# Optimization experiments

Measured on AMD Instinct MI355X. Metric: run time of the kernel, lower is better.

Reference implementation:

```python
import jax, jax.numpy as jnp
import numpy as np

ENC, TAG, LANG, ATT = 512, 512, 512, 256
N, P = 1024, 1024


def setup_inputs() -> dict:
    key = jax.random.key(0)
    ks = jax.random.split(key, 11)
    s = lambda d: 1.0 / np.sqrt(d)
    return {
        "encoder_out": jax.random.normal(ks[0], (1, P, ENC), jnp.float32),
        "decoder_hidden": jax.random.normal(ks[1], (N, TAG), jnp.float32),
        "language_out": jax.random.normal(ks[2], (N, LANG), jnp.float32),
        "We": jax.random.uniform(ks[3], (ATT, ENC), jnp.float32, -s(ENC), s(ENC)),
        "be": jax.random.uniform(ks[4], (ATT,), jnp.float32, -s(ENC), s(ENC)),
        "Wt": jax.random.uniform(ks[5], (ATT, TAG), jnp.float32, -s(TAG), s(TAG)),
        "bt": jax.random.uniform(ks[6], (ATT,), jnp.float32, -s(TAG), s(TAG)),
        "Wl": jax.random.uniform(ks[7], (ATT, LANG), jnp.float32, -s(LANG), s(LANG)),
        "bl": jax.random.uniform(ks[8], (ATT,), jnp.float32, -s(LANG), s(LANG)),
        "Wf": jax.random.uniform(ks[9], (1, ATT), jnp.float32, -s(ATT), s(ATT)),
        "bf": jax.random.uniform(ks[10], (1,), jnp.float32, -s(ATT), s(ATT)),
    }


def reference(encoder_out, decoder_hidden, language_out, We, be, Wt, bt, Wl, bl, Wf, bf):
    # att1: (1, P, A); att2, att3: (N, A)
    att1 = jnp.einsum("bpe,ae->bpa", encoder_out, We) + be
    att2 = decoder_hidden @ Wt.T + bt
    att3 = language_out @ Wl.T + bl
    # broadcast add -> (N, P, A), relu, reduce to scalar score per pixel
    h = jax.nn.relu(att1 + (att2 + att3)[:, None, :])  # (N, P, A)
    att = jnp.einsum("npa,a->np", h, Wf[0]) + bf[0]     # (N, P)
    alpha = jax.nn.softmax(att, axis=1)
    # softmax-weighted sum over pixels -> (N, ENC)
    awe = jnp.einsum("np,pe->ne", alpha, encoder_out[0])
    return awe, alpha
```

## Files before the change

### kernel.cpp

```cpp
#include <hip/hip_runtime.h>
#include <hip/hip_bf16.h>
#include <math.h>

#define ENC 512
#define ATT 256
#define NN 1024
#define PP 1024

typedef __attribute__((ext_vector_type(8))) __bf16 bf16x8;
typedef __attribute__((ext_vector_type(4))) float floatx4;
typedef __attribute__((ext_vector_type(2))) float floatx2;

union LdsVec { uint4 u; bf16x8 v; };

__device__ __forceinline__ unsigned cvt_pk(float lo, float hi) {
    union { __hip_bfloat162 h; unsigned u; } x;
    x.h = __float22bfloat162_rn(float2{lo, hi});
    return x.u;
}
__device__ __forceinline__ uint4 cvt8(float4 f0, float4 f1) {
    uint4 r;
    r.x = cvt_pk(f0.x, f0.y); r.y = cvt_pk(f0.z, f0.w);
    r.z = cvt_pk(f1.x, f1.y); r.w = cvt_pk(f1.z, f1.w);
    return r;
}
__device__ __forceinline__ float2 bfpair(unsigned w) {
    union { unsigned u; float f; } lo, hi;
    lo.u = w << 16; hi.u = w & 0xffff0000u;
    return float2{lo.f, hi.f};
}

__device__ __forceinline__ int tile_off(int row, int k) {
    return row * 32 + ((((k >> 3) ^ ((row >> 1) & 3)) & 3) << 3) + (k & 7);
}

__global__ __launch_bounds__(256) void mfma_uv(
    const float* __restrict__ E,  const float* __restrict__ We, const float* __restrict__ be,
    const float* __restrict__ D,  const float* __restrict__ Wt, const float* __restrict__ bt,
    const float* __restrict__ Lg, const float* __restrict__ Wl, const float* __restrict__ bl,
    unsigned short* __restrict__ uT, unsigned short* __restrict__ v1T,
    unsigned short* __restrict__ v2T, unsigned short* __restrict__ ET,
    float* __restrict__ S)
{
    const int tid = threadIdx.x;

    if (blockIdx.z == 3) {
        if (blockIdx.x == 0 && blockIdx.y == 0) {
            const floatx4 z4 = {0.f, 0.f, 0.f, 0.f};
            *(floatx4*)&S[tid * 4] = z4;
        }
        __shared__ unsigned short T[64][72];
        const int k0 = blockIdx.y * 64;
        const int kr = tid >> 2, nc = (tid & 3) * 16;
        const int nr = tid >> 2, kc = (tid & 3) * 16;
        #pragma unroll
        for (int t = 0; t < 2; ++t) {
            const int n0 = (blockIdx.x * 2 + t) * 64;
            const float* ep = E + (size_t)(k0 + kr) * ENC + n0 + nc;
            float4 a = *(const float4*)(ep + 0),  b = *(const float4*)(ep + 4);
            float4 c = *(const float4*)(ep + 8),  d = *(const float4*)(ep + 12);
            if (t) __syncthreads();
            *(uint4*)&T[kr][nc]     = cvt8(a, b);
            *(uint4*)&T[kr][nc + 8] = cvt8(c, d);
            __syncthreads();
            unsigned short tmp[16];
            #pragma unroll
            for (int i = 0; i < 16; ++i) tmp[i] = T[kc + i][nr];
            unsigned short* op = ET + (size_t)(n0 + nr) * PP + k0 + kc;
            *(uint4*)(op)     = *(uint4*)&tmp[0];
            *(uint4*)(op + 8) = *(uint4*)&tmp[8];
        }
        return;
    }

    __shared__ __align__(16) unsigned short As[2][64 * 32];
    __shared__ __align__(16) unsigned short Bs[2][64 * 32];
    const int K = 512;

    const float *A, *B, *bias; unsigned short* out;
    if      (blockIdx.z == 0) { A = E;  B = We; bias = be; out = uT;  }
    else if (blockIdx.z == 1) { A = D;  B = Wt; bias = bt; out = v1T; }
    else                      { A = Lg; B = Wl; bias = bl; out = v2T; }

    const int m0 = blockIdx.y * 64, n0 = blockIdx.x * 64;
    const int wv = tid >> 6, lm = tid & 15, lq = (tid >> 4) & 3;
    const int mb = (wv & 1) * 32, nb = (wv >> 1) * 32;
    const int a0o = tile_off(mb + lm,      lq * 8);
    const int a1o = tile_off(mb + 16 + lm, lq * 8);
    const int b0o = tile_off(nb + lm,      lq * 8);
    const int b1o = tile_off(nb + 16 + lm, lq * 8);

    const int row = tid >> 2, kseg = tid & 3;
    const int soff = tile_off(row, kseg * 8);
    const float* Ap = A + (size_t)(m0 + row) * K + kseg * 8;
    const float* Bp = B + (size_t)(n0 + row) * K + kseg * 8;

    floatx4 acc[2][2];
    const floatx4 zero = {0.f, 0.f, 0.f, 0.f};
    acc[0][0] = zero; acc[0][1] = zero; acc[1][0] = zero; acc[1][1] = zero;

    float4 pa0 = *(const float4*)(Ap), pa1 = *(const float4*)(Ap + 4);
    float4 pb0 = *(const float4*)(Bp), pb1 = *(const float4*)(Bp + 4);

    for (int k0 = 0; k0 < K; k0 += 32) {
        const int buf = (k0 >> 5) & 1;
        *(uint4*)&As[buf][soff] = cvt8(pa0, pa1);
        *(uint4*)&Bs[buf][soff] = cvt8(pb0, pb1);
        __syncthreads();
        if (k0 + 32 < K) {
            pa0 = *(const float4*)(Ap + k0 + 32); pa1 = *(const float4*)(Ap + k0 + 36);
            pb0 = *(const float4*)(Bp + k0 + 32); pb1 = *(const float4*)(Bp + k0 + 36);
        }
        LdsVec fa0, fa1, fb0, fb1;
        fa0.u = *(const uint4*)&As[buf][a0o];
        fa1.u = *(const uint4*)&As[buf][a1o];
        fb0.u = *(const uint4*)&Bs[buf][b0o];
        fb1.u = *(const uint4*)&Bs[buf][b1o];
        acc[0][0] = __builtin_amdgcn_mfma_f32_16x16x32_bf16(fa0.v, fb0.v, acc[0][0], 0, 0, 0);
        acc[0][1] = __builtin_amdgcn_mfma_f32_16x16x32_bf16(fa0.v, fb1.v, acc[0][1], 0, 0, 0);
        acc[1][0] = __builtin_amdgcn_mfma_f32_16x16x32_bf16(fa1.v, fb0.v, acc[1][0], 0, 0, 0);
        acc[1][1] = __builtin_amdgcn_mfma_f32_16x16x32_bf16(fa1.v, fb1.v, acc[1][1], 0, 0, 0);
    }

    #pragma unroll
    for (int s = 0; s < 2; ++s) {
        const int col = n0 + nb + s * 16 + lm;
        const float bsum = bias[col];
        #pragma unroll
        for (int t = 0; t < 2; ++t) {
            const int mbase = m0 + mb + t * 16 + lq * 4;
            uint2 o;
            o.x = cvt_pk(acc[t][s][0] + bsum, acc[t][s][1] + bsum);
            o.y = cvt_pk(acc[t][s][2] + bsum, acc[t][s][3] + bsum);
            *(uint2*)&out[(size_t)col * NN + mbase] = o;
        }
    }
}

__global__ __launch_bounds__(256) void att_exp(
    const unsigned short* __restrict__ uT, const unsigned short* __restrict__ v1T,
    const unsigned short* __restrict__ v2T,
    const float* __restrict__ Wf,
    unsigned short* __restrict__ expv, float* __restrict__ S)
{
    __shared__ float us[32][68];
    __shared__ float vs[32][68];
    __shared__ float wfs[ATT];
    const int tid = threadIdx.x;
    wfs[tid] = Wf[tid];
    const int p0 = blockIdx.x * 64, n0 = blockIdx.y * 64;
    const int rowS = tid >> 3, cS = (tid & 7) * 8;
    const int tx = tid & 15, ty = tid >> 4;

    floatx2 acc[4][2];
    const floatx2 z2 = {0.f, 0.f};
    #pragma unroll
    for (int j = 0; j < 4; ++j) { acc[j][0] = z2; acc[j][1] = z2; }

    for (int ac = 0; ac < ATT; ac += 32) {
        __syncthreads();
        {
            const size_t arow_g = (size_t)(ac + rowS) * NN;
            uint4 ua = *(const uint4*)(uT + arow_g + p0 + cS);
            float* ud = &us[rowS][cS];
            float2 c;
            c = bfpair(ua.x); ud[0] = c.x; ud[1] = c.y;
            c = bfpair(ua.y); ud[2] = c.x; ud[3] = c.y;
            c = bfpair(ua.z); ud[4] = c.x; ud[5] = c.y;
            c = bfpair(ua.w); ud[6] = c.x; ud[7] = c.y;
            uint4 va = *(const uint4*)(v1T + arow_g + n0 + cS);
            uint4 vb = *(const uint4*)(v2T + arow_g + n0 + cS);
            float* vd = &vs[rowS][cS];
            float2 a0, b0;
            a0 = bfpair(va.x); b0 = bfpair(vb.x); vd[0] = a0.x + b0.x; vd[1] = a0.y + b0.y;
            a0 = bfpair(va.y); b0 = bfpair(vb.y); vd[2] = a0.x + b0.x; vd[3] = a0.y + b0.y;
            a0 = bfpair(va.z); b0 = bfpair(vb.z); vd[4] = a0.x + b0.x; vd[5] = a0.y + b0.y;
            a0 = bfpair(va.w); b0 = bfpair(vb.w); vd[6] = a0.x + b0.x; vd[7] = a0.y + b0.y;
        }
        __syncthreads();
        #pragma unroll
        for (int a = 0; a < 32; ++a) {
            float4 u4 = *(const float4*)&us[a][tx * 4];
            float4 v4 = *(const float4*)&vs[a][ty * 4];
            const float w = wfs[ac + a];
            floatx2 ulo = {u4.x, u4.y}, uhi = {u4.z, u4.w};
            const float vv[4] = {v4.x, v4.y, v4.z, v4.w};
            #pragma unroll
            for (int j = 0; j < 4; ++j) {
                floatx2 t0 = __builtin_elementwise_max(ulo + vv[j], z2);
                floatx2 t1 = __builtin_elementwise_max(uhi + vv[j], z2);
                acc[j][0] = t0 * w + acc[j][0];
                acc[j][1] = t1 * w + acc[j][1];
            }
        }
    }

    #pragma unroll
    for (int j = 0; j < 4; ++j) {
        const int n = n0 + ty * 4 + j;
        float e0 = __expf(acc[j][0].x), e1 = __expf(acc[j][0].y);
        float e2 = __expf(acc[j][1].x), e3 = __expf(acc[j][1].y);
        float s = (e0 + e1) + (e2 + e3);
        s += __shfl_xor(s, 1, 64);
        s += __shfl_xor(s, 2, 64);
        s += __shfl_xor(s, 4, 64);
        s += __shfl_xor(s, 8, 64);
        if (tx == 0) atomicAdd(&S[n], s);
        uint2 pk;
        pk.x = cvt_pk(e0, e1);
        pk.y = cvt_pk(e2, e3);
        *(uint2*)&expv[(size_t)n * PP + p0 + tx * 4] = pk;
    }
}

__global__ __launch_bounds__(256) void mfma_awe(
    const unsigned short* __restrict__ expv,
    const unsigned short* __restrict__ ET,
    const float* __restrict__ S,
    float* __restrict__ awe, float* __restrict__ alpha)
{
    __shared__ __align__(16) unsigned short As[2][32 * 32];
    __shared__ __align__(16) unsigned short Bs[2][64 * 32];
    const int tid = threadIdx.x;
    const int K = PP;
    const int m0 = blockIdx.y * 32, n0 = blockIdx.x * 64;
    const int wv = tid >> 6, lm = tid & 15, lq = (tid >> 4) & 3;
    const int mw = (wv & 1) * 16, nw = (wv >> 1) * 32;
    const int a0o = tile_off(mw + lm,      lq * 8);
    const int b0o = tile_off(nw + lm,      lq * 8);
    const int b1o = tile_off(nw + 16 + lm, lq * 8);

    const int rowA = tid >> 3, kcA = (tid & 7) * 4;
    const int rowB = tid >> 2, kcB = (tid & 3) * 8;
    const int aoff = tile_off(rowA, kcA);
    const int boff = tile_off(rowB, kcB);
    const unsigned short* Ap = expv + (size_t)(m0 + rowA) * PP + kcA;
    const unsigned short* Bp = ET + (size_t)(n0 + rowB) * PP + kcB;

    floatx4 acc[2];
    const floatx4 zero = {0.f, 0.f, 0.f, 0.f};
    acc[0] = zero; acc[1] = zero;

    uint2 pa = *(const uint2*)Ap;
    uint4 pb = *(const uint4*)Bp;

    for (int k0 = 0; k0 < K; k0 += 32) {
        const int buf = (k0 >> 5) & 1;
        *(uint2*)&As[buf][aoff] = pa;
        *(uint4*)&Bs[buf][boff] = pb;
        __syncthreads();
        if (k0 + 32 < K) {
            pa = *(const uint2*)(Ap + k0 + 32);
            pb = *(const uint4*)(Bp + k0 + 32);
        }
        LdsVec fa, fb0, fb1;
        fa.u  = *(const uint4*)&As[buf][a0o];
        fb0.u = *(const uint4*)&Bs[buf][b0o];
        fb1.u = *(const uint4*)&Bs[buf][b1o];
        acc[0] = __builtin_amdgcn_mfma_f32_16x16x32_bf16(fa.v, fb0.v, acc[0], 0, 0, 0);
        acc[1] = __builtin_amdgcn_mfma_f32_16x16x32_bf16(fa.v, fb1.v, acc[1], 0, 0, 0);
    }

    float inv[4];
    #pragma unroll
    for (int r = 0; r < 4; ++r) inv[r] = 1.0f / S[m0 + mw + lq * 4 + r];

    #pragma unroll
    for (int s = 0; s < 2; ++s) {
        const int col = n0 + nw + s * 16 + lm;
        #pragma unroll
        for (int r = 0; r < 4; ++r)
            awe[(size_t)(m0 + mw + lq * 4 + r) * ENC + col] = acc[s][r] * inv[r];
    }

    if (blockIdx.x == 0) {
        const int r = tid >> 3;
        const int c0 = (tid & 7) * 128;
        const int rown = m0 + r;
        const float rinv = 1.0f / S[rown];
        const unsigned short* ep = expv + (size_t)rown * PP + c0;
        float* ap = alpha + (size_t)rown * PP + c0;
        #pragma unroll
        for (int i = 0; i < 128; i += 8) {
            uint4 w = *(const uint4*)&ep[i];
            float2 c0v = bfpair(w.x), c1v = bfpair(w.y);
            float2 c2v = bfpair(w.z), c3v = bfpair(w.w);
            float4 o0, o1;
            o0.x = c0v.x * rinv; o0.y = c0v.y * rinv;
            o0.z = c1v.x * rinv; o0.w = c1v.y * rinv;
            o1.x = c2v.x * rinv; o1.y = c2v.y * rinv;
            o1.z = c3v.x * rinv; o1.w = c3v.y * rinv;
            *(float4*)&ap[i]     = o0;
            *(float4*)&ap[i + 4] = o1;
        }
    }
}

extern "C" void kernel_launch(void* const* d_in, const int* in_sizes, int n_in,
                              void* d_out, int out_size, void* d_ws, size_t ws_size,
                              hipStream_t stream)
{
    const float* encoder = (const float*)d_in[0];
    const float* dec     = (const float*)d_in[1];
    const float* lang    = (const float*)d_in[2];
    const float* We      = (const float*)d_in[3];
    const float* be      = (const float*)d_in[4];
    const float* Wt      = (const float*)d_in[5];
    const float* bt      = (const float*)d_in[6];
    const float* Wl      = (const float*)d_in[7];
    const float* bl      = (const float*)d_in[8];
    const float* Wf      = (const float*)d_in[9];

    unsigned short* uT   = (unsigned short*)d_ws;
    unsigned short* v1T  = uT  + ATT * NN;
    unsigned short* v2T  = v1T + ATT * NN;
    unsigned short* ET   = v2T + ATT * NN;
    unsigned short* expv = ET + (size_t)ENC * PP;
    float* S             = (float*)(expv + (size_t)NN * PP);

    float* awe   = (float*)d_out;
    float* alpha = (float*)d_out + NN * ENC;

    mfma_uv<<<dim3(4, 16, 4), 256, 0, stream>>>(
        encoder, We, be, dec, Wt, bt, lang, Wl, bl, uT, v1T, v2T, ET, S);
    att_exp<<<dim3(PP / 64, NN / 64), 256, 0, stream>>>(uT, v1T, v2T, Wf, expv, S);
    mfma_awe<<<dim3(ENC / 64, NN / 32), 256, 0, stream>>>(expv, ET, S, awe, alpha);
}
```

Measured before the change: 143.3 us.

## Compute softmax row sums inside awe GEMM instead of atomics in att_exp

Drops the shuffle reduction and global atomicAdd of softmax denominators from att_exp, along with the zeroing of S in the first kernel. The awe kernel now accumulates each row's sum from the bf16 exp values it already loads into LDS. Sums are reduced with shuffles into shared memory, and the alpha normalization is spread across all x-blocks rather than done only by blockIdx.x==0. The trade-off is that the sum uses bf16-rounded exps, and every x-block recomputes the same row sums.

```diff
diff --git a/kernel.cpp b/kernel.cpp
--- a/kernel.cpp
+++ b/kernel.cpp
@@ -39,16 +39,11 @@
     const float* __restrict__ D,  const float* __restrict__ Wt, const float* __restrict__ bt,
     const float* __restrict__ Lg, const float* __restrict__ Wl, const float* __restrict__ bl,
     unsigned short* __restrict__ uT, unsigned short* __restrict__ v1T,
-    unsigned short* __restrict__ v2T, unsigned short* __restrict__ ET,
-    float* __restrict__ S)
+    unsigned short* __restrict__ v2T, unsigned short* __restrict__ ET)
 {
     const int tid = threadIdx.x;
 
     if (blockIdx.z == 3) {
-        if (blockIdx.x == 0 && blockIdx.y == 0) {
-            const floatx4 z4 = {0.f, 0.f, 0.f, 0.f};
-            *(floatx4*)&S[tid * 4] = z4;
-        }
         __shared__ unsigned short T[64][72];
         const int k0 = blockIdx.y * 64;
         const int kr = tid >> 2, nc = (tid & 3) * 16;
@@ -141,7 +136,7 @@
     const unsigned short* __restrict__ uT, const unsigned short* __restrict__ v1T,
     const unsigned short* __restrict__ v2T,
     const float* __restrict__ Wf,
-    unsigned short* __restrict__ expv, float* __restrict__ S)
+    unsigned short* __restrict__ expv)
 {
     __shared__ float us[32][68];
     __shared__ float vs[32][68];
@@ -198,17 +193,9 @@
     #pragma unroll
     for (int j = 0; j < 4; ++j) {
         const int n = n0 + ty * 4 + j;
-        float e0 = __expf(acc[j][0].x), e1 = __expf(acc[j][0].y);
-        float e2 = __expf(acc[j][1].x), e3 = __expf(acc[j][1].y);
-        float s = (e0 + e1) + (e2 + e3);
-        s += __shfl_xor(s, 1, 64);
-        s += __shfl_xor(s, 2, 64);
-        s += __shfl_xor(s, 4, 64);
-        s += __shfl_xor(s, 8, 64);
-        if (tx == 0) atomicAdd(&S[n], s);
         uint2 pk;
-        pk.x = cvt_pk(e0, e1);
-        pk.y = cvt_pk(e2, e3);
+        pk.x = cvt_pk(__expf(acc[j][0].x), __expf(acc[j][0].y));
+        pk.y = cvt_pk(__expf(acc[j][1].x), __expf(acc[j][1].y));
         *(uint2*)&expv[(size_t)n * PP + p0 + tx * 4] = pk;
     }
 }
@@ -216,11 +203,11 @@
 __global__ __launch_bounds__(256) void mfma_awe(
     const unsigned short* __restrict__ expv,
     const unsigned short* __restrict__ ET,
-    const float* __restrict__ S,
     float* __restrict__ awe, float* __restrict__ alpha)
 {
     __shared__ __align__(16) unsigned short As[2][32 * 32];
     __shared__ __align__(16) unsigned short Bs[2][64 * 32];
+    __shared__ float Sl[32];
     const int tid = threadIdx.x;
     const int K = PP;
     const int m0 = blockIdx.y * 32, n0 = blockIdx.x * 64;
@@ -230,7 +217,7 @@
     const int b0o = tile_off(nw + lm,      lq * 8);
     const int b1o = tile_off(nw + 16 + lm, lq * 8);
 
-    const int rowA = tid >> 3, kcA = (tid & 7) * 4;
+    const int rowA = tid >> 3, t8 = tid & 7, kcA = t8 * 4;
     const int rowB = tid >> 2, kcB = (tid & 3) * 8;
     const int aoff = tile_off(rowA, kcA);
     const int boff = tile_off(rowB, kcB);
@@ -240,6 +227,7 @@
     floatx4 acc[2];
     const floatx4 zero = {0.f, 0.f, 0.f, 0.f};
     acc[0] = zero; acc[1] = zero;
+    float s_part = 0.f;
 
     uint2 pa = *(const uint2*)Ap;
     uint4 pb = *(const uint4*)Bp;
@@ -248,6 +236,10 @@
         const int buf = (k0 >> 5) & 1;
         *(uint2*)&As[buf][aoff] = pa;
         *(uint4*)&Bs[buf][boff] = pb;
+        {
+            float2 x = bfpair(pa.x), y = bfpair(pa.y);
+            s_part += (x.x + x.y) + (y.x + y.y);
+        }
         __syncthreads();
         if (k0 + 32 < K) {
             pa = *(const uint2*)(Ap + k0 + 32);
@@ -261,9 +253,15 @@
         acc[1] = __builtin_amdgcn_mfma_f32_16x16x32_bf16(fa.v, fb1.v, acc[1], 0, 0, 0);
     }
 
+    s_part += __shfl_xor(s_part, 1, 64);
+    s_part += __shfl_xor(s_part, 2, 64);
+    s_part += __shfl_xor(s_part, 4, 64);
+    if (t8 == 0) Sl[rowA] = s_part;
+    __syncthreads();
+
     float inv[4];
     #pragma unroll
-    for (int r = 0; r < 4; ++r) inv[r] = 1.0f / S[m0 + mw + lq * 4 + r];
+    for (int r = 0; r < 4; ++r) inv[r] = 1.0f / Sl[mw + lq * 4 + r];
 
     #pragma unroll
     for (int s = 0; s < 2; ++s) {
@@ -273,26 +271,29 @@
             awe[(size_t)(m0 + mw + lq * 4 + r) * ENC + col] = acc[s][r] * inv[r];
     }
 
-    if (blockIdx.x == 0) {
-        const int r = tid >> 3;
-        const int c0 = (tid & 7) * 128;
-        const int rown = m0 + r;
-        const float rinv = 1.0f / S[rown];
+    {
+        const int lr = blockIdx.x * 4 + (tid >> 6);
+        const int rown = m0 + lr;
+        const float rinv = 1.0f / Sl[lr];
+        const int c0 = (tid & 63) * 16;
         const unsigned short* ep = expv + (size_t)rown * PP + c0;
         float* ap = alpha + (size_t)rown * PP + c0;
-        #pragma unroll
-        for (int i = 0; i < 128; i += 8) {
-            uint4 w = *(const uint4*)&ep[i];
-            float2 c0v = bfpair(w.x), c1v = bfpair(w.y);
-            float2 c2v = bfpair(w.z), c3v = bfpair(w.w);
-            float4 o0, o1;
-            o0.x = c0v.x * rinv; o0.y = c0v.y * rinv;
-            o0.z = c1v.x * rinv; o0.w = c1v.y * rinv;
-            o1.x = c2v.x * rinv; o1.y = c2v.y * rinv;
-            o1.z = c3v.x * rinv; o1.w = c3v.y * rinv;
-            *(float4*)&ap[i]     = o0;
-            *(float4*)&ap[i + 4] = o1;
-        }
+        uint4 w0 = *(const uint4*)ep;
+        uint4 w1 = *(const uint4*)(ep + 8);
+        float2 c01, c23;
+        float4 o;
+        c01 = bfpair(w0.x); c23 = bfpair(w0.y);
+        o.x = c01.x * rinv; o.y = c01.y * rinv; o.z = c23.x * rinv; o.w = c23.y * rinv;
+        *(float4*)&ap[0] = o;
+        c01 = bfpair(w0.z); c23 = bfpair(w0.w);
+        o.x = c01.x * rinv; o.y = c01.y * rinv; o.z = c23.x * rinv; o.w = c23.y * rinv;
+        *(float4*)&ap[4] = o;
+        c01 = bfpair(w1.x); c23 = bfpair(w1.y);
+        o.x = c01.x * rinv; o.y = c01.y * rinv; o.z = c23.x * rinv; o.w = c23.y * rinv;
+        *(float4*)&ap[8] = o;
+        c01 = bfpair(w1.z); c23 = bfpair(w1.w);
+        o.x = c01.x * rinv; o.y = c01.y * rinv; o.z = c23.x * rinv; o.w = c23.y * rinv;
+        *(float4*)&ap[12] = o;
     }
 }
 
@@ -316,13 +317,12 @@
     unsigned short* v2T  = v1T + ATT * NN;
     unsigned short* ET   = v2T + ATT * NN;
     unsigned short* expv = ET + (size_t)ENC * PP;
-    float* S             = (float*)(expv + (size_t)NN * PP);
 
     float* awe   = (float*)d_out;
     float* alpha = (float*)d_out + NN * ENC;
 
     mfma_uv<<<dim3(4, 16, 4), 256, 0, stream>>>(
-        encoder, We, be, dec, Wt, bt, lang, Wl, bl, uT, v1T, v2T, ET, S);
-    att_exp<<<dim3(PP / 64, NN / 64), 256, 0, stream>>>(uT, v1T, v2T, Wf, expv, S);
-    mfma_awe<<<dim3(ENC / 64, NN / 32), 256, 0, stream>>>(expv, ET, S, awe, alpha);
-}
+        encoder, We, be, dec, Wt, bt, lang, Wl, bl, uT, v1T, v2T, ET);
+    att_exp<<<dim3(PP / 64, NN / 64), 256, 0, stream>>>(uT, v1T, v2T, Wf, expv);
+    mfma_awe<<<dim3(ENC / 64, NN / 32), 256, 0, stream>>>(expv, ET, awe, alpha);
+}
```

Measured after the change: 131.5 us. 8.2% less time.
